# Performance work log

Measured on AMD Instinct MI355X. Metric: run time of the kernel, lower is better.

The kernel has to match this reference:

```python
import jax, jax.numpy as jnp
import numpy as np

D_EMBD = 1024
N_HEADS = 16
D_HEAD = D_EMBD // N_HEADS
BS, T = 2, 2048


def setup_inputs() -> dict:
    key = jax.random.key(0)
    ks = jax.random.split(key, 5)
    s1 = 1.0 / np.sqrt(D_EMBD)
    x = jax.random.normal(ks[0], (BS, T, D_EMBD), dtype=jnp.float32)
    # dense1: Linear(d_embd, 3*d_embd); stored as [in, out] matmul matrix
    W1 = jax.random.uniform(ks[1], (D_EMBD, 3 * D_EMBD), jnp.float32, -s1, s1)
    b1 = jax.random.uniform(ks[2], (3 * D_EMBD,), jnp.float32, -s1, s1)
    # dense2: Linear(d_embd, d_embd)
    W2 = jax.random.uniform(ks[3], (D_EMBD, D_EMBD), jnp.float32, -s1, s1)
    b2 = jax.random.uniform(ks[4], (D_EMBD,), jnp.float32, -s1, s1)
    return {"x": x, "W1": W1, "b1": b1, "W2": W2, "b2": b2}


def reference(x, W1, b1, W2, b2):
    bs, t, d = x.shape
    kqv = x @ W1 + b1                               # [b, t, 3d]
    # torch.chunk order in source: k, q, v
    k, q, v = jnp.split(kqv, 3, axis=-1)
    def heads(z):  # [b, t, (h d)] -> [b, h, t, d]
        return z.reshape(bs, t, N_HEADS, D_HEAD).transpose(0, 2, 1, 3)
    k, q, v = heads(k), heads(q), heads(v)
    scale = 1.0 / np.sqrt(D_HEAD).astype(np.float32)
    attn = jnp.einsum('bhtd,bhsd->bhts', q, k) * scale   # [b, h, t, t]
    causal = jnp.tril(jnp.ones((t, t), dtype=bool))
    attn = jnp.where(causal, attn, -jnp.inf)
    attn = jax.nn.softmax(attn, axis=-1)
    out = jnp.einsum('bhts,bhsd->bhtd', attn, v)         # [b, h, t, d]
    out = out.transpose(0, 2, 1, 3).reshape(bs, t, d)    # [b, t, (h d)]
    return out @ W2 + b2
```

## Files before the change

kernel.cpp:

```cpp
#include <hip/hip_runtime.h>

typedef unsigned short ushort_t;
typedef short bf16x8 __attribute__((ext_vector_type(8)));
typedef short bf16x4 __attribute__((ext_vector_type(4)));
typedef float f32x4 __attribute__((ext_vector_type(4)));

__device__ __forceinline__ unsigned f2bf(float f) {
    union { float f; unsigned u; } c; c.f = f;
    unsigned u = c.u;
    u += 0x7FFFu + ((u >> 16) & 1u);
    return u >> 16;
}

__device__ __forceinline__ float bf2f(unsigned lo16) {
    union { unsigned u; float f; } c; c.u = lo16 << 16; return c.f;
}

__device__ __forceinline__ unsigned pack_trunc(float a, float b) {
    union { float f; unsigned u; } ca, cb; ca.f = a; cb.f = b;
    return (ca.u >> 16) | (cb.u & 0xFFFF0000u);
}

__device__ __forceinline__ void async16(const ushort_t* g, ushort_t* l) {
    __builtin_amdgcn_global_load_lds(
        (const __attribute__((address_space(1))) unsigned int*)g,
        (__attribute__((address_space(3))) unsigned int*)l, 16, 0, 0);
}

__global__ __launch_bounds__(256) void prep_kernel(
    const float* __restrict__ x, const float* __restrict__ W1, const float* __restrict__ W2,
    ushort_t* __restrict__ xb, ushort_t* __restrict__ w1t, ushort_t* __restrict__ w2t) {
    __shared__ float tile[64][65];
    const int tid = threadIdx.x;
    const int bid = blockIdx.x;
    if (bid < 2048) {
        const int i = (bid * 256 + tid) * 8;
        const float4 a = *(const float4*)(x + i);
        const float4 b = *(const float4*)(x + i + 4);
        uint4 pk;
        pk.x = f2bf(a.x) | (f2bf(a.y) << 16);
        pk.y = f2bf(a.z) | (f2bf(a.w) << 16);
        pk.z = f2bf(b.x) | (f2bf(b.y) << 16);
        pk.w = f2bf(b.z) | (f2bf(b.w) << 16);
        *(uint4*)(xb + i) = pk;
        return;
    }
    const float* src; ushort_t* dst; int R, C, r0, c0;
    if (bid < 2816) {
        const int t = bid - 2048;
        src = W1; dst = w1t; R = 1024; C = 3072;
        c0 = (t % 48) * 64; r0 = (t / 48) * 64;
    } else {
        const int t = bid - 2816;
        src = W2; dst = w2t; R = 1024; C = 1024;
        c0 = (t & 15) * 64; r0 = (t >> 4) * 64;
    }
    const int rr = tid >> 4, cc = (tid & 15) * 4;
#pragma unroll
    for (int i = 0; i < 4; ++i) {
        const float4 v = *(const float4*)(src + (size_t)(r0 + rr + 16 * i) * C + c0 + cc);
        tile[rr + 16 * i][cc]     = v.x;
        tile[rr + 16 * i][cc + 1] = v.y;
        tile[rr + 16 * i][cc + 2] = v.z;
        tile[rr + 16 * i][cc + 3] = v.w;
    }
    __syncthreads();
#pragma unroll
    for (int i = 0; i < 4; ++i) {
        const int orow = rr + 16 * i;
        uint2 pk;
        pk.x = f2bf(tile[cc][orow])     | (f2bf(tile[cc + 1][orow]) << 16);
        pk.y = f2bf(tile[cc + 2][orow]) | (f2bf(tile[cc + 3][orow]) << 16);
        *(uint2*)(dst + (size_t)(c0 + orow) * R + r0 + cc) = pk;
    }
}

__device__ __forceinline__ void gemm_core_128(const ushort_t* __restrict__ A,
                                              const ushort_t* __restrict__ B,
                                              int m0, int n0,
                                              ushort_t* As, ushort_t* Bs,
                                              f32x4 acc[4][4], int tid) {
    const int w = tid >> 6, lane = tid & 63, quad = lane >> 4, l16 = lane & 15;
    const int wrow = (w >> 1) * 64, wcol = (w & 1) * 64;
    const ushort_t* Ab = A + (size_t)m0 * 1024;
    const ushort_t* Bb = B + (size_t)n0 * 1024;
    for (int kt = 0; kt < 32; ++kt) {
        const int k0 = kt * 32;
#pragma unroll
        for (int c = 0; c < 2; ++c) {
            const int e = c * 2048 + tid * 8;
            const int row = e >> 5, col = e & 31;
            async16(Ab + (size_t)row * 1024 + k0 + col, As + e);
            async16(Bb + (size_t)row * 1024 + k0 + col, Bs + e);
        }
        __syncthreads();
        bf16x8 af[4], bfr[4];
#pragma unroll
        for (int i = 0; i < 4; ++i) {
            af[i]  = *(const bf16x8*)(As + (wrow + i * 16 + l16) * 32 + quad * 8);
            bfr[i] = *(const bf16x8*)(Bs + (wcol + i * 16 + l16) * 32 + quad * 8);
        }
#pragma unroll
        for (int mi = 0; mi < 4; ++mi)
#pragma unroll
            for (int ni = 0; ni < 4; ++ni)
                acc[mi][ni] = __builtin_amdgcn_mfma_f32_16x16x32_bf16(
                    af[mi], bfr[ni], acc[mi][ni], 0, 0, 0);
        __syncthreads();
    }
}

__global__ __launch_bounds__(256) void gemm_qkv_kernel(
    const ushort_t* __restrict__ xb, const ushort_t* __restrict__ w1t,
    const float* __restrict__ b1,
    ushort_t* __restrict__ kb, ushort_t* __restrict__ qb, ushort_t* __restrict__ vb) {
    __shared__ __attribute__((aligned(16))) ushort_t As[128 * 32];
    __shared__ __attribute__((aligned(16))) ushort_t Bs[128 * 32];
    const int tid = threadIdx.x;
    const int m0 = blockIdx.y * 128, n0 = blockIdx.x * 128;
    f32x4 acc[4][4];
    const f32x4 z4 = {0.f, 0.f, 0.f, 0.f};
#pragma unroll
    for (int i = 0; i < 4; ++i)
#pragma unroll
        for (int j = 0; j < 4; ++j) acc[i][j] = z4;
    gemm_core_128(xb, w1t, m0, n0, As, Bs, acc, tid);

    const int w = tid >> 6, lane = tid & 63, quad = lane >> 4, l16 = lane & 15;
    const int wrow = (w >> 1) * 64, wcol = (w & 1) * 64;
    const int chunk = n0 >> 10;
#pragma unroll
    for (int mi = 0; mi < 4; ++mi) {
#pragma unroll
        for (int ni = 0; ni < 4; ++ni) {
            const int cg = n0 + wcol + ni * 16 + l16;
            const float bias = b1[cg];
            const int hc = cg & 1023;
            const int h = hc >> 6, d = hc & 63;
#pragma unroll
            for (int r = 0; r < 4; ++r) {
                const int rg = m0 + wrow + mi * 16 + quad * 4 + r;
                const int bb = rg >> 11, tt = rg & 2047;
                const int bh = bb * 16 + h;
                const float v = acc[mi][ni][r] + bias;
                if (chunk == 0)
                    kb[((size_t)bh * 2048 + tt) * 64 + d] = (ushort_t)f2bf(v);
                else if (chunk == 1)
                    qb[((size_t)bh * 2048 + tt) * 64 + d] = (ushort_t)f2bf(v * 0.1803368801f);
                else
                    vb[((size_t)bh * 64 + d) * 2048 + tt] = (ushort_t)f2bf(v);
            }
        }
    }
}

__device__ __constant__ int4 ATTN_SCHED[24] = {
    {15, 0, 16, 22}, {14, 0, 16, 20}, {13, 0, 16, 18}, {12, 0, 16, 16},
    {11, 0, 16, 14}, {10, 0, 16, 12}, { 9, 0, 16, 10}, { 8, 0, 16,  8},
    { 7, 0, 16,  7}, {15, 16, 16, 23}, { 6, 0, 14,  6}, {14, 16, 14, 21},
    { 5, 0, 12,  5}, {13, 16, 12, 19}, { 4, 0, 10,  4}, {12, 16, 10, 17},
    { 3, 0,  8,  3}, {11, 16,  8, 15}, { 2, 0,  6,  2}, {10, 16,  6, 13},
    { 1, 0,  4,  1}, { 9, 16,  4, 11}, { 0, 0,  2,  0}, { 8, 16,  2,  9}
};

__global__ __launch_bounds__(256) void attn_kernel(
    const ushort_t* __restrict__ qb, const ushort_t* __restrict__ kb,
    const ushort_t* __restrict__ vb,
    ushort_t* __restrict__ Opart, float* __restrict__ lpart) {
    __shared__ __attribute__((aligned(16))) ushort_t Ks[2][64][72];
    __shared__ __attribute__((aligned(16))) ushort_t Vs[2][64][72];

    const int tid = threadIdx.x;
    const int w = tid >> 6, lane = tid & 63, quad = lane >> 4, l16 = lane & 15;
    const int bh = blockIdx.x;
    const int4 sc = ATTN_SCHED[blockIdx.y];
    const int qtile = sc.x, k0 = sc.y, kcnt = sc.z;
    const int slot = bh * 24 + sc.w;
    const int q0 = qtile * 128;
    const int q0w = q0 + w * 32;
    const int kend = k0 + kcnt;
    const float NEG_INF = -__builtin_inff();

    const ushort_t* Q = qb + (size_t)bh * (2048 * 64);
    const ushort_t* K = kb + (size_t)bh * (2048 * 64);
    const ushort_t* V = vb + (size_t)bh * (64 * 2048);

    bf16x8 aq[2][2];
#pragma unroll
    for (int u = 0; u < 2; ++u)
#pragma unroll
        for (int kh = 0; kh < 2; ++kh)
            aq[u][kh] = *(const bf16x8*)(Q + (size_t)(q0w + u * 16 + l16) * 64 + kh * 32 + quad * 8);

    const int srow = tid >> 2, scol = (tid & 3) * 16;

    uint4 kr0, kr1, vr0, vr1;
    {
        const uint4* kp = (const uint4*)(K + (size_t)(k0 * 64 + srow) * 64 + scol);
        kr0 = kp[0]; kr1 = kp[1];
        const uint4* vp = (const uint4*)(V + (size_t)srow * 2048 + k0 * 64 + scol);
        vr0 = vp[0]; vr1 = vp[1];
    }

    float l_i[2] = {0.f, 0.f};
    f32x4 o[2][4];
    const f32x4 z4 = {0.f, 0.f, 0.f, 0.f};
#pragma unroll
    for (int u = 0; u < 2; ++u)
#pragma unroll
        for (int d = 0; d < 4; ++d) o[u][d] = z4;

    for (int kt = k0; kt < kend; ++kt) {
        const int cur = kt & 1;
        *(uint4*)&Ks[cur][srow][scol]     = kr0;
        *(uint4*)&Ks[cur][srow][scol + 8] = kr1;
        *(uint4*)&Vs[cur][srow][scol]     = vr0;
        *(uint4*)&Vs[cur][srow][scol + 8] = vr1;
        __syncthreads();
        if (kt + 1 < kend) {
            const uint4* kp = (const uint4*)(K + (size_t)((kt + 1) * 64 + srow) * 64 + scol);
            kr0 = kp[0]; kr1 = kp[1];
            const uint4* vp = (const uint4*)(V + (size_t)srow * 2048 + (kt + 1) * 64 + scol);
            vr0 = vp[0]; vr1 = vp[1];
        }
        if (kt * 64 >= q0w + 32) continue;

        bf16x8 af[4][2];
#pragma unroll
        for (int ni = 0; ni < 4; ++ni)
#pragma unroll
            for (int kh = 0; kh < 2; ++kh)
                af[ni][kh] = *(const bf16x8*)&Ks[cur][ni * 16 + l16][kh * 32 + quad * 8];
        f32x4 st[2][4];
#pragma unroll
        for (int u = 0; u < 2; ++u)
#pragma unroll
            for (int ni = 0; ni < 4; ++ni) {
                f32x4 acc = z4;
                acc = __builtin_amdgcn_mfma_f32_16x16x32_bf16(af[ni][0], aq[u][0], acc, 0, 0, 0);
                acc = __builtin_amdgcn_mfma_f32_16x16x32_bf16(af[ni][1], aq[u][1], acc, 0, 0, 0);
                st[u][ni] = acc;
            }
        if (kt >= 2 * qtile) {
#pragma unroll
            for (int u = 0; u < 2; ++u)
#pragma unroll
                for (int ni = 0; ni < 4; ++ni)
#pragma unroll
                    for (int r = 0; r < 4; ++r) {
                        const int s = kt * 64 + ni * 16 + quad * 4 + r;
                        const int q = q0w + u * 16 + l16;
                        if (s > q) st[u][ni][r] = NEG_INF;
                    }
        }
        bf16x4 ph[2][4];
#pragma unroll
        for (int u = 0; u < 2; ++u) {
            float p[4][4], rs = 0.f;
#pragma unroll
            for (int ni = 0; ni < 4; ++ni)
#pragma unroll
                for (int r = 0; r < 4; ++r) {
                    p[ni][r] = __builtin_amdgcn_exp2f(st[u][ni][r]);
                    rs += p[ni][r];
                }
            l_i[u] += rs;
#pragma unroll
            for (int ni = 0; ni < 4; ++ni) {
                union { bf16x4 v; uint2 uu; } pk;
                pk.uu.x = pack_trunc(p[ni][0], p[ni][1]);
                pk.uu.y = pack_trunc(p[ni][2], p[ni][3]);
                ph[u][ni] = pk.v;
            }
        }
#pragma unroll
        for (int ni = 0; ni < 4; ++ni)
#pragma unroll
            for (int dt = 0; dt < 4; ++dt) {
                const bf16x4 av = *(const bf16x4*)&Vs[cur][dt * 16 + l16][ni * 16 + quad * 4];
                o[0][dt] = __builtin_amdgcn_mfma_f32_16x16x16bf16_1k(av, ph[0][ni], o[0][dt], 0, 0, 0);
                o[1][dt] = __builtin_amdgcn_mfma_f32_16x16x16bf16_1k(av, ph[1][ni], o[1][dt], 0, 0, 0);
            }
    }
#pragma unroll
    for (int u = 0; u < 2; ++u) {
        float l = l_i[u];
        l += __shfl_xor(l, 16);
        l += __shfl_xor(l, 32);
        const int row = w * 32 + u * 16 + l16;
        if (quad == 0) lpart[slot * 128 + row] = l;
#pragma unroll
        for (int dt = 0; dt < 4; ++dt) {
            uint2 pk;
            pk.x = f2bf(o[u][dt][0]) | (f2bf(o[u][dt][1]) << 16);
            pk.y = f2bf(o[u][dt][2]) | (f2bf(o[u][dt][3]) << 16);
            *(uint2*)&Opart[(size_t)slot * 8192 + row * 64 + dt * 16 + quad * 4] = pk;
        }
    }
}

__global__ __launch_bounds__(256) void merge_kernel(
    const ushort_t* __restrict__ Opart, const float* __restrict__ lpart,
    ushort_t* __restrict__ aout) {
    __shared__ float inv[128];
    const int bh = blockIdx.x, q = blockIdx.y;
    int s0, n;
    if (q < 8) { s0 = bh * 24 + q; n = 1; }
    else       { s0 = bh * 24 + 8 + 2 * (q - 8); n = 2; }
    const int t = threadIdx.x;
    if (t < 128) {
        float l = lpart[s0 * 128 + t];
        if (n == 2) l += lpart[(s0 + 1) * 128 + t];
        inv[t] = 1.0f / l;
    }
    __syncthreads();
    const int b = bh >> 4, h = bh & 15;
#pragma unroll
    for (int i = 0; i < 8; ++i) {
        const int e = i * 1024 + t * 4;
        const int row = e >> 6, d = e & 63;
        const uint2 a = *(const uint2*)&Opart[(size_t)s0 * 8192 + e];
        float v0 = bf2f(a.x & 0xFFFFu), v1 = bf2f(a.x >> 16);
        float v2 = bf2f(a.y & 0xFFFFu), v3 = bf2f(a.y >> 16);
        if (n == 2) {
            const uint2 bb = *(const uint2*)&Opart[(size_t)(s0 + 1) * 8192 + e];
            v0 += bf2f(bb.x & 0xFFFFu); v1 += bf2f(bb.x >> 16);
            v2 += bf2f(bb.y & 0xFFFFu); v3 += bf2f(bb.y >> 16);
        }
        const float iv = inv[row];
        uint2 opk;
        opk.x = f2bf(v0 * iv) | (f2bf(v1 * iv) << 16);
        opk.y = f2bf(v2 * iv) | (f2bf(v3 * iv) << 16);
        *(uint2*)&aout[(size_t)(b * 2048 + q * 128 + row) * 1024 + h * 64 + d] = opk;
    }
}

__global__ __launch_bounds__(256) void gemm_out_kernel(
    const ushort_t* __restrict__ ab, const ushort_t* __restrict__ w2t,
    const float* __restrict__ b2, float* __restrict__ out) {
    __shared__ __attribute__((aligned(16))) ushort_t As[128 * 32];
    __shared__ __attribute__((aligned(16))) ushort_t Bs[64 * 32];
    const int tid = threadIdx.x;
    const int w = tid >> 6, lane = tid & 63, quad = lane >> 4, l16 = lane & 15;
    const int n0 = blockIdx.x * 64, m0 = blockIdx.y * 128;
    f32x4 acc[2][4];
    const f32x4 z4 = {0.f, 0.f, 0.f, 0.f};
#pragma unroll
    for (int i = 0; i < 2; ++i)
#pragma unroll
        for (int j = 0; j < 4; ++j) acc[i][j] = z4;
    const ushort_t* Ab = ab + (size_t)m0 * 1024;
    const ushort_t* Bb = w2t + (size_t)n0 * 1024;
    for (int kt = 0; kt < 32; ++kt) {
        const int k0 = kt * 32;
        {
            const int e = tid * 8;
            async16(Ab + (size_t)(e >> 5) * 1024 + k0 + (e & 31), As + e);
            const int e2 = 2048 + e;
            async16(Ab + (size_t)(e2 >> 5) * 1024 + k0 + (e2 & 31), As + e2);
            async16(Bb + (size_t)(e >> 5) * 1024 + k0 + (e & 31), Bs + e);
        }
        __syncthreads();
        bf16x8 af[2], bfr[4];
#pragma unroll
        for (int mi = 0; mi < 2; ++mi)
            af[mi] = *(const bf16x8*)(As + (w * 32 + mi * 16 + l16) * 32 + quad * 8);
#pragma unroll
        for (int ni = 0; ni < 4; ++ni)
            bfr[ni] = *(const bf16x8*)(Bs + (ni * 16 + l16) * 32 + quad * 8);
#pragma unroll
        for (int mi = 0; mi < 2; ++mi)
#pragma unroll
            for (int ni = 0; ni < 4; ++ni)
                acc[mi][ni] = __builtin_amdgcn_mfma_f32_16x16x32_bf16(
                    af[mi], bfr[ni], acc[mi][ni], 0, 0, 0);
        __syncthreads();
    }
#pragma unroll
    for (int mi = 0; mi < 2; ++mi) {
#pragma unroll
        for (int ni = 0; ni < 4; ++ni) {
            const int cg = n0 + ni * 16 + l16;
            const float bias = b2[cg];
#pragma unroll
            for (int r = 0; r < 4; ++r) {
                const int rg = m0 + w * 32 + mi * 16 + quad * 4 + r;
                out[(size_t)rg * 1024 + cg] = acc[mi][ni][r] + bias;
            }
        }
    }
}

extern "C" void kernel_launch(void* const* d_in, const int* in_sizes, int n_in,
                              void* d_out, int out_size, void* d_ws, size_t ws_size,
                              hipStream_t stream) {
    const float* x  = (const float*)d_in[0];
    const float* W1 = (const float*)d_in[1];
    const float* b1 = (const float*)d_in[2];
    const float* W2 = (const float*)d_in[3];
    const float* b2 = (const float*)d_in[4];
    float* out = (float*)d_out;

    char* ws = (char*)d_ws;
    const size_t MB = 1024 * 1024;
    ushort_t* xb  = (ushort_t*)(ws);
    ushort_t* w1t = (ushort_t*)(ws + 8 * MB);
    ushort_t* w2t = (ushort_t*)(ws + 14 * MB);
    ushort_t* kb  = (ushort_t*)(ws + 16 * MB);
    ushort_t* qb  = (ushort_t*)(ws + 24 * MB);
    ushort_t* vb  = (ushort_t*)(ws + 32 * MB);
    ushort_t* ao  = (ushort_t*)(ws + 40 * MB);
    ushort_t* Opart = (ushort_t*)(ws);
    float*    lpart = (float*)(ws + 13 * MB);

    prep_kernel<<<3072, 256, 0, stream>>>(x, W1, W2, xb, w1t, w2t);
    gemm_qkv_kernel<<<dim3(24, 32), 256, 0, stream>>>(xb, w1t, b1, kb, qb, vb);
    attn_kernel<<<dim3(32, 24), 256, 0, stream>>>(qb, kb, vb, Opart, lpart);
    merge_kernel<<<dim3(32, 16), 256, 0, stream>>>(Opart, lpart, ao);
    gemm_out_kernel<<<dim3(16, 32), 256, 0, stream>>>(ao, w2t, b2, out);
}
```

Baseline: 185.6 us.

## Rebalance attention split schedule and double GEMM K-step to 64

The attention schedule now splits only the eight heaviest query tiles into two balanced key-range halves. The other eight tiles are processed whole and write normalized output directly to the attention buffer, so the merge kernel only combines pairs for tiles 8-15 and launches half as many blocks. Both GEMM kernels also load a 64-wide K slab per barrier pair instead of 32, halving the number of synchronizations at the cost of double the shared memory per block. This cuts partial-output traffic and merge work, but may change occupancy in the GEMMs.

```diff
diff --git a/kernel.cpp b/kernel.cpp
--- a/kernel.cpp
+++ b/kernel.cpp
@@ -75,37 +75,42 @@
     }
 }
 
-__device__ __forceinline__ void gemm_core_128(const ushort_t* __restrict__ A,
-                                              const ushort_t* __restrict__ B,
-                                              int m0, int n0,
-                                              ushort_t* As, ushort_t* Bs,
-                                              f32x4 acc[4][4], int tid) {
+__device__ __forceinline__ void gemm_core_bk64(const ushort_t* __restrict__ A,
+                                               const ushort_t* __restrict__ B,
+                                               int m0, int n0,
+                                               ushort_t* As, ushort_t* Bs,
+                                               f32x4 acc[4][4], int tid) {
     const int w = tid >> 6, lane = tid & 63, quad = lane >> 4, l16 = lane & 15;
     const int wrow = (w >> 1) * 64, wcol = (w & 1) * 64;
     const ushort_t* Ab = A + (size_t)m0 * 1024;
     const ushort_t* Bb = B + (size_t)n0 * 1024;
-    for (int kt = 0; kt < 32; ++kt) {
-        const int k0 = kt * 32;
-#pragma unroll
-        for (int c = 0; c < 2; ++c) {
-            const int e = c * 2048 + tid * 8;
-            const int row = e >> 5, col = e & 31;
-            async16(Ab + (size_t)row * 1024 + k0 + col, As + e);
-            async16(Bb + (size_t)row * 1024 + k0 + col, Bs + e);
-        }
+    for (int kt = 0; kt < 16; ++kt) {
+        const int k0 = kt * 64;
+#pragma unroll
+        for (int kh = 0; kh < 2; ++kh)
+#pragma unroll
+            for (int c = 0; c < 2; ++c) {
+                const int e = c * 2048 + tid * 8;
+                const int row = e >> 5, col = e & 31;
+                async16(Ab + (size_t)row * 1024 + k0 + kh * 32 + col, As + kh * 4096 + e);
+                async16(Bb + (size_t)row * 1024 + k0 + kh * 32 + col, Bs + kh * 4096 + e);
+            }
         __syncthreads();
-        bf16x8 af[4], bfr[4];
-#pragma unroll
-        for (int i = 0; i < 4; ++i) {
-            af[i]  = *(const bf16x8*)(As + (wrow + i * 16 + l16) * 32 + quad * 8);
-            bfr[i] = *(const bf16x8*)(Bs + (wcol + i * 16 + l16) * 32 + quad * 8);
-        }
-#pragma unroll
-        for (int mi = 0; mi < 4; ++mi)
-#pragma unroll
-            for (int ni = 0; ni < 4; ++ni)
-                acc[mi][ni] = __builtin_amdgcn_mfma_f32_16x16x32_bf16(
-                    af[mi], bfr[ni], acc[mi][ni], 0, 0, 0);
+#pragma unroll
+        for (int kh = 0; kh < 2; ++kh) {
+            bf16x8 af[4], bfr[4];
+#pragma unroll
+            for (int i = 0; i < 4; ++i) {
+                af[i]  = *(const bf16x8*)(As + kh * 4096 + (wrow + i * 16 + l16) * 32 + quad * 8);
+                bfr[i] = *(const bf16x8*)(Bs + kh * 4096 + (wcol + i * 16 + l16) * 32 + quad * 8);
+            }
+#pragma unroll
+            for (int mi = 0; mi < 4; ++mi)
+#pragma unroll
+                for (int ni = 0; ni < 4; ++ni)
+                    acc[mi][ni] = __builtin_amdgcn_mfma_f32_16x16x32_bf16(
+                        af[mi], bfr[ni], acc[mi][ni], 0, 0, 0);
+        }
         __syncthreads();
     }
 }
@@ -114,8 +119,8 @@
     const ushort_t* __restrict__ xb, const ushort_t* __restrict__ w1t,
     const float* __restrict__ b1,
     ushort_t* __restrict__ kb, ushort_t* __restrict__ qb, ushort_t* __restrict__ vb) {
-    __shared__ __attribute__((aligned(16))) ushort_t As[128 * 32];
-    __shared__ __attribute__((aligned(16))) ushort_t Bs[128 * 32];
+    __shared__ __attribute__((aligned(16))) ushort_t As[2 * 128 * 32];
+    __shared__ __attribute__((aligned(16))) ushort_t Bs[2 * 128 * 32];
     const int tid = threadIdx.x;
     const int m0 = blockIdx.y * 128, n0 = blockIdx.x * 128;
     f32x4 acc[4][4];
@@ -124,7 +129,7 @@
     for (int i = 0; i < 4; ++i)
 #pragma unroll
         for (int j = 0; j < 4; ++j) acc[i][j] = z4;
-    gemm_core_128(xb, w1t, m0, n0, As, Bs, acc, tid);
+    gemm_core_bk64(xb, w1t, m0, n0, As, Bs, acc, tid);
 
     const int w = tid >> 6, lane = tid & 63, quad = lane >> 4, l16 = lane & 15;
     const int wrow = (w >> 1) * 64, wcol = (w & 1) * 64;
@@ -155,18 +160,22 @@
 }
 
 __device__ __constant__ int4 ATTN_SCHED[24] = {
-    {15, 0, 16, 22}, {14, 0, 16, 20}, {13, 0, 16, 18}, {12, 0, 16, 16},
-    {11, 0, 16, 14}, {10, 0, 16, 12}, { 9, 0, 16, 10}, { 8, 0, 16,  8},
-    { 7, 0, 16,  7}, {15, 16, 16, 23}, { 6, 0, 14,  6}, {14, 16, 14, 21},
-    { 5, 0, 12,  5}, {13, 16, 12, 19}, { 4, 0, 10,  4}, {12, 16, 10, 17},
-    { 3, 0,  8,  3}, {11, 16,  8, 15}, { 2, 0,  6,  2}, {10, 16,  6, 13},
-    { 1, 0,  4,  1}, { 9, 16,  4, 11}, { 0, 0,  2,  0}, { 8, 16,  2,  9}
+    {15,  0, 16, 14}, {15, 16, 16, 15}, { 7,  0, 16, -1},
+    {14,  0, 15, 12}, {14, 15, 15, 13},
+    {13,  0, 14, 10}, {13, 14, 14, 11}, { 6,  0, 14, -1},
+    {12,  0, 13,  8}, {12, 13, 13,  9},
+    {11,  0, 12,  6}, {11, 12, 12,  7}, { 5,  0, 12, -1},
+    {10,  0, 11,  4}, {10, 11, 11,  5},
+    { 9,  0, 10,  2}, { 9, 10, 10,  3}, { 4,  0, 10, -1},
+    { 8,  0,  9,  0}, { 8,  9,  9,  1},
+    { 3,  0,  8, -1}, { 2,  0,  6, -1}, { 1,  0,  4, -1}, { 0,  0,  2, -1}
 };
 
 __global__ __launch_bounds__(256) void attn_kernel(
     const ushort_t* __restrict__ qb, const ushort_t* __restrict__ kb,
     const ushort_t* __restrict__ vb,
-    ushort_t* __restrict__ Opart, float* __restrict__ lpart) {
+    ushort_t* __restrict__ Opart, float* __restrict__ lpart,
+    ushort_t* __restrict__ aout) {
     __shared__ __attribute__((aligned(16))) ushort_t Ks[2][64][72];
     __shared__ __attribute__((aligned(16))) ushort_t Vs[2][64][72];
 
@@ -174,8 +183,7 @@
     const int w = tid >> 6, lane = tid & 63, quad = lane >> 4, l16 = lane & 15;
     const int bh = blockIdx.x;
     const int4 sc = ATTN_SCHED[blockIdx.y];
-    const int qtile = sc.x, k0 = sc.y, kcnt = sc.z;
-    const int slot = bh * 24 + sc.w;
+    const int qtile = sc.x, k0 = sc.y, kcnt = sc.z, slot_ofs = sc.w;
     const int q0 = qtile * 128;
     const int q0w = q0 + w * 32;
     const int kend = k0 + kcnt;
@@ -282,19 +290,39 @@
                 o[1][dt] = __builtin_amdgcn_mfma_f32_16x16x16bf16_1k(av, ph[1][ni], o[1][dt], 0, 0, 0);
             }
     }
-#pragma unroll
-    for (int u = 0; u < 2; ++u) {
-        float l = l_i[u];
-        l += __shfl_xor(l, 16);
-        l += __shfl_xor(l, 32);
-        const int row = w * 32 + u * 16 + l16;
-        if (quad == 0) lpart[slot * 128 + row] = l;
-#pragma unroll
-        for (int dt = 0; dt < 4; ++dt) {
-            uint2 pk;
-            pk.x = f2bf(o[u][dt][0]) | (f2bf(o[u][dt][1]) << 16);
-            pk.y = f2bf(o[u][dt][2]) | (f2bf(o[u][dt][3]) << 16);
-            *(uint2*)&Opart[(size_t)slot * 8192 + row * 64 + dt * 16 + quad * 4] = pk;
+    if (slot_ofs < 0) {
+        const int b = bh >> 4, h = bh & 15;
+#pragma unroll
+        for (int u = 0; u < 2; ++u) {
+            float l = l_i[u];
+            l += __shfl_xor(l, 16);
+            l += __shfl_xor(l, 32);
+            const float inv = 1.0f / l;
+            const int q = q0w + u * 16 + l16;
+#pragma unroll
+            for (int dt = 0; dt < 4; ++dt) {
+                uint2 pk;
+                pk.x = f2bf(o[u][dt][0] * inv) | (f2bf(o[u][dt][1] * inv) << 16);
+                pk.y = f2bf(o[u][dt][2] * inv) | (f2bf(o[u][dt][3] * inv) << 16);
+                *(uint2*)&aout[(size_t)(b * 2048 + q) * 1024 + h * 64 + dt * 16 + quad * 4] = pk;
+            }
+        }
+    } else {
+        const int slot = bh * 16 + slot_ofs;
+#pragma unroll
+        for (int u = 0; u < 2; ++u) {
+            float l = l_i[u];
+            l += __shfl_xor(l, 16);
+            l += __shfl_xor(l, 32);
+            const int row = w * 32 + u * 16 + l16;
+            if (quad == 0) lpart[slot * 128 + row] = l;
+#pragma unroll
+            for (int dt = 0; dt < 4; ++dt) {
+                uint2 pk;
+                pk.x = f2bf(o[u][dt][0]) | (f2bf(o[u][dt][1]) << 16);
+                pk.y = f2bf(o[u][dt][2]) | (f2bf(o[u][dt][3]) << 16);
+                *(uint2*)&Opart[(size_t)slot * 8192 + row * 64 + dt * 16 + quad * 4] = pk;
+            }
         }
     }
 }
@@ -303,16 +331,11 @@
     const ushort_t* __restrict__ Opart, const float* __restrict__ lpart,
     ushort_t* __restrict__ aout) {
     __shared__ float inv[128];
-    const int bh = blockIdx.x, q = blockIdx.y;
-    int s0, n;
-    if (q < 8) { s0 = bh * 24 + q; n = 1; }
-    else       { s0 = bh * 24 + 8 + 2 * (q - 8); n = 2; }
+    const int bh = blockIdx.x, qtile = 8 + blockIdx.y;
+    const int s0 = bh * 16 + (qtile - 8) * 2;
     const int t = threadIdx.x;
-    if (t < 128) {
-        float l = lpart[s0 * 128 + t];
-        if (n == 2) l += lpart[(s0 + 1) * 128 + t];
-        inv[t] = 1.0f / l;
-    }
+    if (t < 128)
+        inv[t] = 1.0f / (lpart[s0 * 128 + t] + lpart[(s0 + 1) * 128 + t]);
     __syncthreads();
     const int b = bh >> 4, h = bh & 15;
 #pragma unroll
@@ -320,26 +343,24 @@
         const int e = i * 1024 + t * 4;
         const int row = e >> 6, d = e & 63;
         const uint2 a = *(const uint2*)&Opart[(size_t)s0 * 8192 + e];
-        float v0 = bf2f(a.x & 0xFFFFu), v1 = bf2f(a.x >> 16);
-        float v2 = bf2f(a.y & 0xFFFFu), v3 = bf2f(a.y >> 16);
-        if (n == 2) {
-            const uint2 bb = *(const uint2*)&Opart[(size_t)(s0 + 1) * 8192 + e];
-            v0 += bf2f(bb.x & 0xFFFFu); v1 += bf2f(bb.x >> 16);
-            v2 += bf2f(bb.y & 0xFFFFu); v3 += bf2f(bb.y >> 16);
-        }
+        const uint2 bb = *(const uint2*)&Opart[(size_t)(s0 + 1) * 8192 + e];
+        const float v0 = bf2f(a.x & 0xFFFFu) + bf2f(bb.x & 0xFFFFu);
+        const float v1 = bf2f(a.x >> 16)     + bf2f(bb.x >> 16);
+        const float v2 = bf2f(a.y & 0xFFFFu) + bf2f(bb.y & 0xFFFFu);
+        const float v3 = bf2f(a.y >> 16)     + bf2f(bb.y >> 16);
         const float iv = inv[row];
         uint2 opk;
         opk.x = f2bf(v0 * iv) | (f2bf(v1 * iv) << 16);
         opk.y = f2bf(v2 * iv) | (f2bf(v3 * iv) << 16);
-        *(uint2*)&aout[(size_t)(b * 2048 + q * 128 + row) * 1024 + h * 64 + d] = opk;
+        *(uint2*)&aout[(size_t)(b * 2048 + qtile * 128 + row) * 1024 + h * 64 + d] = opk;
     }
 }
 
 __global__ __launch_bounds__(256) void gemm_out_kernel(
     const ushort_t* __restrict__ ab, const ushort_t* __restrict__ w2t,
     const float* __restrict__ b2, float* __restrict__ out) {
-    __shared__ __attribute__((aligned(16))) ushort_t As[128 * 32];
-    __shared__ __attribute__((aligned(16))) ushort_t Bs[64 * 32];
+    __shared__ __attribute__((aligned(16))) ushort_t As[2 * 128 * 32];
+    __shared__ __attribute__((aligned(16))) ushort_t Bs[2 * 64 * 32];
     const int tid = threadIdx.x;
     const int w = tid >> 6, lane = tid & 63, quad = lane >> 4, l16 = lane & 15;
     const int n0 = blockIdx.x * 64, m0 = blockIdx.y * 128;
@@ -351,29 +372,33 @@
         for (int j = 0; j < 4; ++j) acc[i][j] = z4;
     const ushort_t* Ab = ab + (size_t)m0 * 1024;
     const ushort_t* Bb = w2t + (size_t)n0 * 1024;
-    for (int kt = 0; kt < 32; ++kt) {
-        const int k0 = kt * 32;
-        {
-            const int e = tid * 8;
-            async16(Ab + (size_t)(e >> 5) * 1024 + k0 + (e & 31), As + e);
-            const int e2 = 2048 + e;
-            async16(Ab + (size_t)(e2 >> 5) * 1024 + k0 + (e2 & 31), As + e2);
-            async16(Bb + (size_t)(e >> 5) * 1024 + k0 + (e & 31), Bs + e);
+    for (int kt = 0; kt < 16; ++kt) {
+        const int k0 = kt * 64;
+#pragma unroll
+        for (int kh = 0; kh < 2; ++kh) {
+            const int e0 = tid * 8;
+            const int e1 = 2048 + e0;
+            async16(Ab + (size_t)(e0 >> 5) * 1024 + k0 + kh * 32 + (e0 & 31), As + kh * 4096 + e0);
+            async16(Ab + (size_t)(e1 >> 5) * 1024 + k0 + kh * 32 + (e1 & 31), As + kh * 4096 + e1);
+            async16(Bb + (size_t)(e0 >> 5) * 1024 + k0 + kh * 32 + (e0 & 31), Bs + kh * 2048 + e0);
         }
         __syncthreads();
-        bf16x8 af[2], bfr[4];
-#pragma unroll
-        for (int mi = 0; mi < 2; ++mi)
-            af[mi] = *(const bf16x8*)(As + (w * 32 + mi * 16 + l16) * 32 + quad * 8);
-#pragma unroll
-        for (int ni = 0; ni < 4; ++ni)
-            bfr[ni] = *(const bf16x8*)(Bs + (ni * 16 + l16) * 32 + quad * 8);
-#pragma unroll
-        for (int mi = 0; mi < 2; ++mi)
+#pragma unroll
+        for (int kh = 0; kh < 2; ++kh) {
+            bf16x8 af[2], bfr[4];
+#pragma unroll
+            for (int mi = 0; mi < 2; ++mi)
+                af[mi] = *(const bf16x8*)(As + kh * 4096 + (w * 32 + mi * 16 + l16) * 32 + quad * 8);
 #pragma unroll
             for (int ni = 0; ni < 4; ++ni)
-                acc[mi][ni] = __builtin_amdgcn_mfma_f32_16x16x32_bf16(
-                    af[mi], bfr[ni], acc[mi][ni], 0, 0, 0);
+                bfr[ni] = *(const bf16x8*)(Bs + kh * 2048 + (ni * 16 + l16) * 32 + quad * 8);
+#pragma unroll
+            for (int mi = 0; mi < 2; ++mi)
+#pragma unroll
+                for (int ni = 0; ni < 4; ++ni)
+                    acc[mi][ni] = __builtin_amdgcn_mfma_f32_16x16x32_bf16(
+                        af[mi], bfr[ni], acc[mi][ni], 0, 0, 0);
+        }
         __syncthreads();
     }
 #pragma unroll
@@ -415,7 +440,7 @@
 
     prep_kernel<<<3072, 256, 0, stream>>>(x, W1, W2, xb, w1t, w2t);
     gemm_qkv_kernel<<<dim3(24, 32), 256, 0, stream>>>(xb, w1t, b1, kb, qb, vb);
-    attn_kernel<<<dim3(32, 24), 256, 0, stream>>>(qb, kb, vb, Opart, lpart);
-    merge_kernel<<<dim3(32, 16), 256, 0, stream>>>(Opart, lpart, ao);
+    attn_kernel<<<dim3(32, 24), 256, 0, stream>>>(qb, kb, vb, Opart, lpart, ao);
+    merge_kernel<<<dim3(32, 8), 256, 0, stream>>>(Opart, lpart, ao);
     gemm_out_kernel<<<dim3(16, 32), 256, 0, stream>>>(ao, w2t, b2, out);
 }
```

Measured after the change: 202.4 us. +9.1%, slower.
